# Kernel optimization log

Measured on AMD Instinct MI355X. Metric: run time of the kernel, lower is better.

## Reference

```python
import jax, jax.numpy as jnp
import numpy as np

B, T, D = 4, 2048, 1024
H, DK = 8, 64
EPS = 1e-6

def _xavier(key, shape):
    fan_in, fan_out = shape[1], shape[0]
    lim = float(np.sqrt(6.0 / (fan_in + fan_out)))
    return jax.random.uniform(key, shape, jnp.float32, -lim, lim)

def setup_inputs() -> dict:
    key = jax.random.key(0)
    ks = jax.random.split(key, 7)
    x = jax.random.normal(ks[0], (B, T, D), jnp.float32)
    W_Q = _xavier(ks[1], (H * DK, D))
    W_K = _xavier(ks[2], (H * DK, D))
    W_V = _xavier(ks[3], (H * DK, D))
    W_g_w = _xavier(ks[4], (H * DK, D))
    W_g_b = jax.random.normal(ks[5], (H * DK,), jnp.float32) * 0.02
    W_O = _xavier(ks[6], (D, H * DK))
    decay_log = jnp.zeros((H,), jnp.float32)
    return {"x": x, "W_Q": W_Q, "W_K": W_K, "W_V": W_V,
            "W_g_w": W_g_w, "W_g_b": W_g_b, "W_O": W_O,
            "decay_log": decay_log}

def _phi(u):
    # ELU + 1 feature map (positive)
    return jax.nn.elu(u) + 1.0

def reference(x, W_Q, W_K, W_V, W_g_w, W_g_b, W_O, decay_log):
    b, t, d = x.shape
    q = _phi((x @ W_Q.T).reshape(b, t, H, DK))
    k = _phi((x @ W_K.T).reshape(b, t, H, DK))
    v = (x @ W_V.T).reshape(b, t, H, DK)
    gamma = jax.nn.sigmoid(decay_log)           # [H]
    g4 = gamma[None, :, None, None]             # [1,H,1,1]
    g3 = gamma[None, :, None]                   # [1,H,1]

    # time-major for scan: [T,B,H,DK]
    qT = jnp.moveaxis(q, 1, 0)
    kT = jnp.moveaxis(k, 1, 0)
    vT = jnp.moveaxis(v, 1, 0)

    S0 = jnp.zeros((b, H, DK, DK), x.dtype)
    z0 = jnp.zeros((b, H, DK), x.dtype)

    def step(carry, inp):
        S, z = carry
        qt, kt, vt = inp
        S = g4 * S + jnp.einsum('bhi,bhj->bhij', kt, vt)
        z = g3 * z + kt
        num = jnp.einsum('bhij,bhi->bhj', S, qt)
        den = jnp.sum(z * qt, axis=-1, keepdims=True) + EPS
        return (S, z), num / den

    _, ys = jax.lax.scan(step, (S0, z0), (qT, kT, vT))  # ys: [T,B,H,DK]
    outputs = jnp.moveaxis(ys, 0, 1)                    # [B,T,H,DK]

    gate = jax.nn.sigmoid(x @ W_g_w.T + W_g_b).reshape(b, t, H, DK)
    y = (outputs * gate).reshape(b, t, H * DK)
    return y @ W_O.T
```

## Files before the change

kernel.cpp:

```cpp
#include <hip/hip_runtime.h>
#include <cstdint>
#include <cstddef>

#define B_   4
#define T_   2048
#define D_   1024
#define H_   8
#define DK_  64
#define HD_  512
#define CH_  64
#define NC_  32
#define EPS_ 1e-6f

typedef __attribute__((ext_vector_type(4))) float f32x4;
typedef __attribute__((ext_vector_type(8))) short s16x8;

__device__ __forceinline__ unsigned short f2bf(float f) {
    unsigned int x = __float_as_uint(f);
    unsigned int r = (x + 0x7FFFu + ((x >> 16) & 1u)) >> 16;
    return (unsigned short)r;
}
__device__ __forceinline__ float bf2f(unsigned short u) {
    return __uint_as_float(((unsigned int)u) << 16);
}
__device__ __forceinline__ void gl_lds16(const unsigned short* g, unsigned short* l) {
    __builtin_amdgcn_global_load_lds(
        (const __attribute__((address_space(1))) unsigned int*)g,
        (__attribute__((address_space(3))) unsigned int*)l, 16, 0, 0);
}

__global__ __launch_bounds__(256) void k_cvt_all(
    const float* __restrict__ x,
    const float* __restrict__ wq, const float* __restrict__ wk,
    const float* __restrict__ wv, const float* __restrict__ wgw,
    const float* __restrict__ wo,
    unsigned short* __restrict__ xb,
    unsigned short* __restrict__ wqb, unsigned short* __restrict__ wkb,
    unsigned short* __restrict__ wvb, unsigned short* __restrict__ wgb,
    unsigned short* __restrict__ wob)
{
    int bid = blockIdx.x;
    const float* src; unsigned short* dst; int idx;
    if (bid < 8192) {
        src = x; dst = xb; idx = bid * 256 + threadIdx.x;
    } else {
        int r = bid - 8192;
        int w = r >> 9;
        idx = (r & 511) * 256 + threadIdx.x;
        switch (w) {
            case 0:  src = wq;  dst = wqb; break;
            case 1:  src = wk;  dst = wkb; break;
            case 2:  src = wv;  dst = wvb; break;
            case 3:  src = wgw; dst = wgb; break;
            default: src = wo;  dst = wob; break;
        }
    }
    float4 v = ((const float4*)src)[idx];
    ushort4 o;
    o.x = f2bf(v.x); o.y = f2bf(v.y); o.z = f2bf(v.z); o.w = f2bf(v.w);
    ((ushort4*)dst)[idx] = o;
}

__global__ __launch_bounds__(512, 2) void k_gemm_qkvg(
    const unsigned short* __restrict__ xb,
    const unsigned short* __restrict__ wqb, const unsigned short* __restrict__ wkb,
    const unsigned short* __restrict__ wvb, const unsigned short* __restrict__ wgb,
    const float* __restrict__ bias,
    unsigned short* __restrict__ qo, unsigned short* __restrict__ ko,
    unsigned short* __restrict__ vo, unsigned short* __restrict__ go)
{
    __shared__ unsigned short As[2][256 * 64];
    __shared__ unsigned short Bs[2][256 * 64];
    const int tid = threadIdx.x;
    const int id  = blockIdx.x;
    const int xcd = id & 7, per = id >> 3;
    const int mtile = xcd * 4 + (per & 3);
    const int ntile = per >> 2;
    const int which = ntile >> 1;
    const int nb    = ntile & 1;
    const int m0    = mtile * 256;
    const int n0    = nb * 256;
    const unsigned short* Wp = (which == 0) ? wqb : (which == 1) ? wkb : (which == 2) ? wvb : wgb;
    unsigned short* Op       = (which == 0) ? qo  : (which == 1) ? ko  : (which == 2) ? vo  : go;
    const int K = D_;
    const int NIT = K / 64;

    const int lane = tid & 63, wave = tid >> 6;
    const int wm = (wave >> 2) * 128, wn = (wave & 3) * 64;
    const int r16 = lane & 15, quad = lane >> 4;
    const int lrow = lane >> 3, lseg = lane & 7;
    const int sseg = lseg ^ lrow;
    const int rx   = r16 & 7;

    f32x4 acc[8][4];
    #pragma unroll
    for (int a = 0; a < 8; a++)
        #pragma unroll
        for (int b = 0; b < 4; b++) acc[a][b] = 0.0f;

    auto stage = [&](int buf, int ko_) {
        #pragma unroll
        for (int i = 0; i < 4; i++) {
            int chunk = wave * 4 + i;
            int row = chunk * 8 + lrow;
            gl_lds16(xb + (size_t)(m0 + row) * K + ko_ + sseg * 8, &As[buf][chunk * 512]);
            gl_lds16(Wp + (size_t)(n0 + row) * K + ko_ + sseg * 8, &Bs[buf][chunk * 512]);
        }
    };

    stage(0, 0);
    for (int it = 0; it < NIT; ++it) {
        if (it + 1 < NIT) {
            stage((it + 1) & 1, (it + 1) * 64);
            asm volatile("s_waitcnt vmcnt(8)" ::: "memory");
        } else {
            asm volatile("s_waitcnt vmcnt(0)" ::: "memory");
        }
        __builtin_amdgcn_s_barrier();
        const int buf = it & 1;
        #pragma unroll
        for (int kk = 0; kk < 64; kk += 32) {
            const int gb_ = kk >> 3;
            s16x8 af[8], bf[4];
            #pragma unroll
            for (int mt = 0; mt < 8; mt++)
                af[mt] = *(const s16x8*)&As[buf][(wm + mt * 16 + r16) * 64 + (((gb_ + quad) ^ rx) << 3)];
            #pragma unroll
            for (int nt = 0; nt < 4; nt++)
                bf[nt] = *(const s16x8*)&Bs[buf][(wn + nt * 16 + r16) * 64 + (((gb_ + quad) ^ rx) << 3)];
            #pragma unroll
            for (int mt = 0; mt < 8; mt++)
                #pragma unroll
                for (int nt = 0; nt < 4; nt++)
                    acc[mt][nt] = __builtin_amdgcn_mfma_f32_16x16x32_bf16(af[mt], bf[nt], acc[mt][nt], 0, 0, 0);
        }
        __builtin_amdgcn_s_barrier();
    }
    #pragma unroll
    for (int mt = 0; mt < 8; mt++) {
        #pragma unroll
        for (int nt = 0; nt < 4; nt++) {
            int col = n0 + wn + nt * 16 + r16;
            float bv = (which == 3) ? bias[col] : 0.0f;
            #pragma unroll
            for (int r = 0; r < 4; r++) {
                int row = m0 + wm + mt * 16 + quad * 4 + r;
                float v = acc[mt][nt][r];
                if (which <= 1)      v = (v > 0.0f) ? v + 1.0f : __builtin_expf(v);
                else if (which == 3) v = 1.0f / (1.0f + __builtin_expf(-(v + bv)));
                Op[(size_t)row * HD_ + col] = f2bf(v);
            }
        }
    }
}

__global__ __launch_bounds__(512, 2) void k_gemm_out(
    const unsigned short* __restrict__ ogb, const unsigned short* __restrict__ wob,
    float* __restrict__ y)
{
    __shared__ unsigned short As[2][256 * 64];
    __shared__ unsigned short Bs[2][128 * 64];
    const int tid = threadIdx.x;
    const int id  = blockIdx.x;
    const int xcd = id & 7, per = id >> 3;
    const int m0 = (xcd * 4 + (per & 3)) * 256;
    const int n0 = (per >> 2) * 128;
    const int K = HD_;
    const int NIT = K / 64;

    const int lane = tid & 63, wave = tid >> 6;
    const int wm = (wave >> 1) * 64, wn = (wave & 1) * 64;
    const int r16 = lane & 15, quad = lane >> 4;
    const int lrow = lane >> 3, lseg = lane & 7;
    const int sseg = lseg ^ lrow;
    const int rx   = r16 & 7;

    f32x4 acc[4][4];
    #pragma unroll
    for (int a = 0; a < 4; a++)
        #pragma unroll
        for (int b = 0; b < 4; b++) acc[a][b] = 0.0f;

    auto stage = [&](int buf, int ko_) {
        #pragma unroll
        for (int i = 0; i < 4; i++) {
            int chunk = wave * 4 + i;
            int row = chunk * 8 + lrow;
            gl_lds16(ogb + (size_t)(m0 + row) * K + ko_ + sseg * 8, &As[buf][chunk * 512]);
        }
        #pragma unroll
        for (int i = 0; i < 2; i++) {
            int chunk = wave * 2 + i;
            int row = chunk * 8 + lrow;
            gl_lds16(wob + (size_t)(n0 + row) * K + ko_ + sseg * 8, &Bs[buf][chunk * 512]);
        }
    };

    stage(0, 0);
    for (int it = 0; it < NIT; ++it) {
        if (it + 1 < NIT) {
            stage((it + 1) & 1, (it + 1) * 64);
            asm volatile("s_waitcnt vmcnt(6)" ::: "memory");
        } else {
            asm volatile("s_waitcnt vmcnt(0)" ::: "memory");
        }
        __builtin_amdgcn_s_barrier();
        const int buf = it & 1;
        #pragma unroll
        for (int kk = 0; kk < 64; kk += 32) {
            const int gb_ = kk >> 3;
            s16x8 af[4], bf[4];
            #pragma unroll
            for (int mt = 0; mt < 4; mt++)
                af[mt] = *(const s16x8*)&As[buf][(wm + mt * 16 + r16) * 64 + (((gb_ + quad) ^ rx) << 3)];
            #pragma unroll
            for (int nt = 0; nt < 4; nt++)
                bf[nt] = *(const s16x8*)&Bs[buf][(wn + nt * 16 + r16) * 64 + (((gb_ + quad) ^ rx) << 3)];
            #pragma unroll
            for (int mt = 0; mt < 4; mt++)
                #pragma unroll
                for (int nt = 0; nt < 4; nt++)
                    acc[mt][nt] = __builtin_amdgcn_mfma_f32_16x16x32_bf16(af[mt], bf[nt], acc[mt][nt], 0, 0, 0);
        }
        __builtin_amdgcn_s_barrier();
    }
    #pragma unroll
    for (int mt = 0; mt < 4; mt++)
        #pragma unroll
        for (int nt = 0; nt < 4; nt++) {
            int col = n0 + wn + nt * 16 + r16;
            #pragma unroll
            for (int r = 0; r < 4; r++) {
                int row = m0 + wm + mt * 16 + quad * 4 + r;
                y[(size_t)row * D_ + col] = acc[mt][nt][r];
            }
        }
}

__global__ __launch_bounds__(256) void k_chunk_sums(
    const unsigned short* __restrict__ Kb, const unsigned short* __restrict__ Vb,
    float* __restrict__ Ssum, float* __restrict__ zsum, const float* __restrict__ decay_log)
{
    __shared__ unsigned short kt[64 * 72];
    __shared__ unsigned short vt[64 * 72];
    const int tid = threadIdx.x;
    const int bc  = blockIdx.x;
    const int c   = bc & (NC_ - 1);
    const int bh  = bc >> 5;
    const int h   = bh & (H_ - 1);
    const int b   = bh >> 3;
    const float g  = 1.0f / (1.0f + __builtin_expf(-decay_log[h]));
    const float lg = __builtin_log2f(g);
    const int t0 = c * CH_;

    #pragma unroll
    for (int e = 0; e < 2; e++) {
        int lid = e * 256 + tid;
        int l = lid >> 3, d0 = (lid & 7) * 8;
        float w = __builtin_exp2f((float)(CH_ - 1 - l) * lg);
        size_t gidx = (size_t)(b * T_ + t0 + l) * HD_ + h * DK_ + d0;
        uint4 kraw = *(const uint4*)(Kb + gidx);
        uint4 vraw = *(const uint4*)(Vb + gidx);
        const unsigned short* kp = (const unsigned short*)&kraw;
        const unsigned short* vp = (const unsigned short*)&vraw;
        #pragma unroll
        for (int j = 0; j < 8; j++) {
            kt[(d0 + j) * 72 + l] = f2bf(bf2f(kp[j]) * w);
            vt[(d0 + j) * 72 + l] = vp[j];
        }
    }
    __syncthreads();

    const int lane = tid & 63, wave = tid >> 6;
    const int r16 = lane & 15, quad = lane >> 4;
    size_t base = (size_t)bc * (DK_ * DK_);

    #pragma unroll
    for (int it = 0; it < 4; it++) {
        f32x4 sacc = 0.0f;
        #pragma unroll
        for (int ks = 0; ks < 2; ks++) {
            s16x8 af  = *(const s16x8*)&vt[(16 * wave + r16) * 72 + ks * 32 + quad * 8];
            s16x8 bf_ = *(const s16x8*)&kt[(16 * it   + r16) * 72 + ks * 32 + quad * 8];
            sacc = __builtin_amdgcn_mfma_f32_16x16x32_bf16(af, bf_, sacc, 0, 0, 0);
        }
        #pragma unroll
        for (int rr = 0; rr < 4; rr++)
            Ssum[base + (size_t)(16 * wave + quad * 4 + rr) * DK_ + 16 * it + r16] = sacc[rr];
    }
    if (tid < DK_) {
        float s = 0.0f;
        #pragma unroll
        for (int l8 = 0; l8 < 8; l8++) {
            uint4 kk = *(const uint4*)&kt[tid * 72 + l8 * 8];
            const unsigned short* kp = (const unsigned short*)&kk;
            #pragma unroll
            for (int e = 0; e < 8; e++) s += bf2f(kp[e]);
        }
        zsum[(size_t)bc * DK_ + tid] = s;
    }
}

__global__ __launch_bounds__(128) void k_chunk_scan(
    float* __restrict__ Ssum, float* __restrict__ zsum, const float* __restrict__ decay_log)
{
    const int tid = threadIdx.x;
    const int grp = blockIdx.x & 31;
    const int bh  = blockIdx.x >> 5;
    const int h   = bh & (H_ - 1);
    const float g  = 1.0f / (1.0f + __builtin_expf(-decay_log[h]));
    const float gC = __builtin_exp2f((float)CH_ * __builtin_log2f(g));
    int elem = grp * 128 + tid;
    float s = 0.0f;
    for (int c = 0; c < NC_; c++) {
        size_t idx = ((size_t)(bh * NC_ + c)) * 4096 + elem;
        float v = Ssum[idx];
        Ssum[idx] = s;
        s = gC * s + v;
    }
    if (grp == 0 && tid < DK_) {
        float z = 0.0f;
        for (int c = 0; c < NC_; c++) {
            size_t idx = ((size_t)(bh * NC_ + c)) * DK_ + tid;
            float v = zsum[idx];
            zsum[idx] = z;
            z = gC * z + v;
        }
    }
}

__global__ __launch_bounds__(256) void k_chunk_out(
    const unsigned short* __restrict__ Qb, const unsigned short* __restrict__ Kb,
    const unsigned short* __restrict__ Vb, const unsigned short* __restrict__ Gb,
    const float* __restrict__ Ssum, const float* __restrict__ zsum,
    unsigned short* __restrict__ OGb, const float* __restrict__ decay_log)
{
    __shared__ unsigned short ql[64 * 72];
    __shared__ unsigned short kl[64 * 72];
    __shared__ unsigned short sT[64 * 72];
    __shared__ unsigned short vt[64 * 72];
    __shared__ unsigned short pl[64 * 72];
    __shared__ float den_l[64];
    __shared__ float zp[64];
    __shared__ float gpow[CH_ + 1];

    const int tid = threadIdx.x;
    const int bc  = blockIdx.x;
    const int c   = bc & (NC_ - 1);
    const int bh  = bc >> 5;
    const int h   = bh & (H_ - 1);
    const int b   = bh >> 3;
    const float g  = 1.0f / (1.0f + __builtin_expf(-decay_log[h]));
    const float lg = __builtin_log2f(g);
    const int t0 = c * CH_;

    if (tid <= CH_) gpow[tid] = __builtin_exp2f((float)tid * lg);
    if (tid < DK_)  zp[tid] = zsum[(size_t)bc * DK_ + tid];

    #pragma unroll
    for (int e = 0; e < 2; e++) {
        int lid = e * 256 + tid;
        int l = lid >> 3, d0 = (lid & 7) * 8;
        size_t gidx = (size_t)(b * T_ + t0 + l) * HD_ + h * DK_ + d0;
        uint4 qraw = *(const uint4*)(Qb + gidx);
        uint4 kraw = *(const uint4*)(Kb + gidx);
        uint4 vraw = *(const uint4*)(Vb + gidx);
        *(uint4*)&ql[l * 72 + d0] = qraw;
        *(uint4*)&kl[l * 72 + d0] = kraw;
        const unsigned short* vp = (const unsigned short*)&vraw;
        #pragma unroll
        for (int j = 0; j < 8; j++) vt[(d0 + j) * 72 + l] = vp[j];
    }
    {
        int j = tid >> 2, seg = tid & 3;
        const float4* src = (const float4*)&Ssum[(size_t)bc * 4096 + (size_t)j * 64 + seg * 16];
        #pragma unroll
        for (int e = 0; e < 4; e++) {
            float4 a4 = src[e];
            ushort4 o;
            o.x = f2bf(a4.x); o.y = f2bf(a4.y); o.z = f2bf(a4.z); o.w = f2bf(a4.w);
            *(ushort4*)&sT[j * 72 + seg * 16 + e * 4] = o;
        }
    }
    __syncthreads();

    const int lane = tid & 63, wave = tid >> 6;
    const int r16 = lane & 15, quad = lane >> 4;
    const int ibase = 16 * wave;

    s16x8 aq[2];
    #pragma unroll
    for (int ks = 0; ks < 2; ks++)
        aq[ks] = *(const s16x8*)&ql[(ibase + r16) * 72 + ks * 32 + quad * 8];

    f32x4 sc4[4];
    #pragma unroll
    for (int lt = 0; lt < 4; lt++) {
        f32x4 s = 0.0f;
        #pragma unroll
        for (int ks = 0; ks < 2; ks++) {
            s16x8 bf_ = *(const s16x8*)&kl[(16 * lt + r16) * 72 + ks * 32 + quad * 8];
            s = __builtin_amdgcn_mfma_f32_16x16x32_bf16(aq[ks], bf_, s, 0, 0, 0);
        }
        sc4[lt] = s;
    }
    float rs[4] = {0.0f, 0.0f, 0.0f, 0.0f};
    #pragma unroll
    for (int lt = 0; lt < 4; lt++) {
        int l = 16 * lt + r16;
        #pragma unroll
        for (int rr = 0; rr < 4; rr++) {
            int i = ibase + quad * 4 + rr;
            float val = (l <= i) ? sc4[lt][rr] * gpow[i - l] : 0.0f;
            unsigned short pb = f2bf(val);
            pl[i * 72 + l] = pb;
            rs[rr] += bf2f(pb);
        }
    }
    #pragma unroll
    for (int rr = 0; rr < 4; rr++) {
        float v_ = rs[rr];
        v_ += __shfl_xor(v_, 1);
        v_ += __shfl_xor(v_, 2);
        v_ += __shfl_xor(v_, 4);
        v_ += __shfl_xor(v_, 8);
        if (r16 == 0) den_l[ibase + quad * 4 + rr] = v_;
    }
    f32x4 og[4];
    #pragma unroll
    for (int jt = 0; jt < 4; jt++) {
        f32x4 o = 0.0f;
        #pragma unroll
        for (int ks = 0; ks < 2; ks++) {
            s16x8 bf_ = *(const s16x8*)&sT[(16 * jt + r16) * 72 + ks * 32 + quad * 8];
            o = __builtin_amdgcn_mfma_f32_16x16x32_bf16(aq[ks], bf_, o, 0, 0, 0);
        }
        #pragma unroll
        for (int rr = 0; rr < 4; rr++)
            o[rr] *= gpow[ibase + quad * 4 + rr + 1];
        og[jt] = o;
    }
    __syncthreads();

    #pragma unroll
    for (int jt = 0; jt < 4; jt++) {
        #pragma unroll
        for (int ks = 0; ks < 2; ks++) {
            s16x8 ap  = *(const s16x8*)&pl[(ibase + r16) * 72 + ks * 32 + quad * 8];
            s16x8 bf_ = *(const s16x8*)&vt[(16 * jt + r16) * 72 + ks * 32 + quad * 8];
            og[jt] = __builtin_amdgcn_mfma_f32_16x16x32_bf16(ap, bf_, og[jt], 0, 0, 0);
        }
    }
    if (tid < DK_) {
        float dp = 0.0f;
        #pragma unroll
        for (int d8 = 0; d8 < 8; d8++) {
            uint4 qq = *(const uint4*)&ql[tid * 72 + d8 * 8];
            const unsigned short* qp = (const unsigned short*)&qq;
            #pragma unroll
            for (int e = 0; e < 8; e++) dp += bf2f(qp[e]) * zp[d8 * 8 + e];
        }
        den_l[tid] += gpow[tid + 1] * dp + EPS_;
    }
    __syncthreads();

    #pragma unroll
    for (int jt = 0; jt < 4; jt++) {
        int j = 16 * jt + r16;
        #pragma unroll
        for (int rr = 0; rr < 4; rr++) {
            int i = ibase + quad * 4 + rr;
            float rcp = 1.0f / den_l[i];
            size_t ga = (size_t)(b * T_ + t0 + i) * HD_ + h * DK_ + j;
            float gate = bf2f(Gb[ga]);
            OGb[ga] = f2bf(og[jt][rr] * rcp * gate);
        }
    }
}

extern "C" void kernel_launch(void* const* d_in, const int* in_sizes, int n_in,
                              void* d_out, int out_size, void* d_ws, size_t ws_size,
                              hipStream_t stream)
{
    (void)in_sizes; (void)n_in; (void)out_size; (void)ws_size;
    const float* x         = (const float*)d_in[0];
    const float* W_Q       = (const float*)d_in[1];
    const float* W_K       = (const float*)d_in[2];
    const float* W_V       = (const float*)d_in[3];
    const float* W_gw      = (const float*)d_in[4];
    const float* W_gb      = (const float*)d_in[5];
    const float* W_O       = (const float*)d_in[6];
    const float* decay_log = (const float*)d_in[7];
    float* y = (float*)d_out;

    char* ws = (char*)d_ws;
    size_t off = 0;
    auto alloc = [&](size_t bytes) { void* p = ws + off; off += (bytes + 255) & ~(size_t)255; return p; };
    unsigned short* xb   = (unsigned short*)alloc((size_t)B_ * T_ * D_ * 2);
    unsigned short* wqb  = (unsigned short*)alloc((size_t)HD_ * D_ * 2);
    unsigned short* wkb  = (unsigned short*)alloc((size_t)HD_ * D_ * 2);
    unsigned short* wvb  = (unsigned short*)alloc((size_t)HD_ * D_ * 2);
    unsigned short* wgb  = (unsigned short*)alloc((size_t)HD_ * D_ * 2);
    unsigned short* wob  = (unsigned short*)alloc((size_t)D_ * HD_ * 2);
    unsigned short* qb   = (unsigned short*)alloc((size_t)B_ * T_ * HD_ * 2);
    unsigned short* kb   = (unsigned short*)alloc((size_t)B_ * T_ * HD_ * 2);
    unsigned short* vb   = (unsigned short*)alloc((size_t)B_ * T_ * HD_ * 2);
    unsigned short* gb   = (unsigned short*)alloc((size_t)B_ * T_ * HD_ * 2);
    unsigned short* ogb  = (unsigned short*)alloc((size_t)B_ * T_ * HD_ * 2);
    float* Ssum = (float*)alloc((size_t)B_ * H_ * NC_ * DK_ * DK_ * 4);
    float* zsum = (float*)alloc((size_t)B_ * H_ * NC_ * DK_ * 4);

    k_cvt_all<<<8192 + 5 * 512, 256, 0, stream>>>(x, W_Q, W_K, W_V, W_gw, W_O,
                                                  xb, wqb, wkb, wvb, wgb, wob);
    k_gemm_qkvg<<<256, 512, 0, stream>>>(xb, wqb, wkb, wvb, wgb, W_gb, qb, kb, vb, gb);
    k_chunk_sums<<<B_ * H_ * NC_, 256, 0, stream>>>(kb, vb, Ssum, zsum, decay_log);
    k_chunk_scan<<<B_ * H_ * NC_, 128, 0, stream>>>(Ssum, zsum, decay_log);
    k_chunk_out<<<B_ * H_ * NC_, 256, 0, stream>>>(qb, kb, vb, gb, Ssum, zsum, ogb, decay_log);
    k_gemm_out<<<256, 512, 0, stream>>>(ogb, wob, y);
}
```

Before: 197.9 us.

## Fuse chunk sums, scan, and output into one cooperative kernel with grid syncs

Merges the three chunked linear-attention kernels into a single cooperative launch of 512 blocks, each handling two chunks, separated by grid-wide syncs. The scan phase spreads across all threads of the grid. This removes two kernel launches and their inter-kernel gaps, at the cost of grid.sync overhead and a grid limited to co-resident blocks (two per CU via launch bounds).

New measurement: 442.7 us. 124% more time.

```diff
diff --git a/kernel.cpp b/kernel.cpp
--- a/kernel.cpp
+++ b/kernel.cpp
@@ -1,6 +1,9 @@
 #include <hip/hip_runtime.h>
+#include <hip/hip_cooperative_groups.h>
 #include <cstdint>
 #include <cstddef>
+
+namespace cg = cooperative_groups;
 
 #define B_   4
 #define T_   2048
@@ -237,243 +240,247 @@
         }
 }
 
-__global__ __launch_bounds__(256) void k_chunk_sums(
-    const unsigned short* __restrict__ Kb, const unsigned short* __restrict__ Vb,
-    float* __restrict__ Ssum, float* __restrict__ zsum, const float* __restrict__ decay_log)
+__global__ __launch_bounds__(256, 2) void k_chunk_all(
+    const unsigned short* __restrict__ Qb, const unsigned short* __restrict__ Kb,
+    const unsigned short* __restrict__ Vb, const unsigned short* __restrict__ Gb,
+    float* __restrict__ Ssum, float* __restrict__ zsum,
+    unsigned short* __restrict__ OGb, const float* __restrict__ decay_log)
 {
     __shared__ unsigned short kt[64 * 72];
     __shared__ unsigned short vt[64 * 72];
-    const int tid = threadIdx.x;
-    const int bc  = blockIdx.x;
-    const int c   = bc & (NC_ - 1);
-    const int bh  = bc >> 5;
-    const int h   = bh & (H_ - 1);
-    const int b   = bh >> 3;
-    const float g  = 1.0f / (1.0f + __builtin_expf(-decay_log[h]));
-    const float lg = __builtin_log2f(g);
-    const int t0 = c * CH_;
-
-    #pragma unroll
-    for (int e = 0; e < 2; e++) {
-        int lid = e * 256 + tid;
-        int l = lid >> 3, d0 = (lid & 7) * 8;
-        float w = __builtin_exp2f((float)(CH_ - 1 - l) * lg);
-        size_t gidx = (size_t)(b * T_ + t0 + l) * HD_ + h * DK_ + d0;
-        uint4 kraw = *(const uint4*)(Kb + gidx);
-        uint4 vraw = *(const uint4*)(Vb + gidx);
-        const unsigned short* kp = (const unsigned short*)&kraw;
-        const unsigned short* vp = (const unsigned short*)&vraw;
-        #pragma unroll
-        for (int j = 0; j < 8; j++) {
-            kt[(d0 + j) * 72 + l] = f2bf(bf2f(kp[j]) * w);
-            vt[(d0 + j) * 72 + l] = vp[j];
-        }
-    }
-    __syncthreads();
-
-    const int lane = tid & 63, wave = tid >> 6;
-    const int r16 = lane & 15, quad = lane >> 4;
-    size_t base = (size_t)bc * (DK_ * DK_);
-
-    #pragma unroll
-    for (int it = 0; it < 4; it++) {
-        f32x4 sacc = 0.0f;
-        #pragma unroll
-        for (int ks = 0; ks < 2; ks++) {
-            s16x8 af  = *(const s16x8*)&vt[(16 * wave + r16) * 72 + ks * 32 + quad * 8];
-            s16x8 bf_ = *(const s16x8*)&kt[(16 * it   + r16) * 72 + ks * 32 + quad * 8];
-            sacc = __builtin_amdgcn_mfma_f32_16x16x32_bf16(af, bf_, sacc, 0, 0, 0);
-        }
-        #pragma unroll
-        for (int rr = 0; rr < 4; rr++)
-            Ssum[base + (size_t)(16 * wave + quad * 4 + rr) * DK_ + 16 * it + r16] = sacc[rr];
-    }
-    if (tid < DK_) {
-        float s = 0.0f;
-        #pragma unroll
-        for (int l8 = 0; l8 < 8; l8++) {
-            uint4 kk = *(const uint4*)&kt[tid * 72 + l8 * 8];
-            const unsigned short* kp = (const unsigned short*)&kk;
-            #pragma unroll
-            for (int e = 0; e < 8; e++) s += bf2f(kp[e]);
-        }
-        zsum[(size_t)bc * DK_ + tid] = s;
-    }
-}
-
-__global__ __launch_bounds__(128) void k_chunk_scan(
-    float* __restrict__ Ssum, float* __restrict__ zsum, const float* __restrict__ decay_log)
-{
-    const int tid = threadIdx.x;
-    const int grp = blockIdx.x & 31;
-    const int bh  = blockIdx.x >> 5;
-    const int h   = bh & (H_ - 1);
-    const float g  = 1.0f / (1.0f + __builtin_expf(-decay_log[h]));
-    const float gC = __builtin_exp2f((float)CH_ * __builtin_log2f(g));
-    int elem = grp * 128 + tid;
-    float s = 0.0f;
-    for (int c = 0; c < NC_; c++) {
-        size_t idx = ((size_t)(bh * NC_ + c)) * 4096 + elem;
-        float v = Ssum[idx];
-        Ssum[idx] = s;
-        s = gC * s + v;
-    }
-    if (grp == 0 && tid < DK_) {
-        float z = 0.0f;
-        for (int c = 0; c < NC_; c++) {
-            size_t idx = ((size_t)(bh * NC_ + c)) * DK_ + tid;
-            float v = zsum[idx];
-            zsum[idx] = z;
-            z = gC * z + v;
-        }
-    }
-}
-
-__global__ __launch_bounds__(256) void k_chunk_out(
-    const unsigned short* __restrict__ Qb, const unsigned short* __restrict__ Kb,
-    const unsigned short* __restrict__ Vb, const unsigned short* __restrict__ Gb,
-    const float* __restrict__ Ssum, const float* __restrict__ zsum,
-    unsigned short* __restrict__ OGb, const float* __restrict__ decay_log)
-{
     __shared__ unsigned short ql[64 * 72];
     __shared__ unsigned short kl[64 * 72];
     __shared__ unsigned short sT[64 * 72];
-    __shared__ unsigned short vt[64 * 72];
     __shared__ unsigned short pl[64 * 72];
     __shared__ float den_l[64];
     __shared__ float zp[64];
     __shared__ float gpow[CH_ + 1];
 
     const int tid = threadIdx.x;
-    const int bc  = blockIdx.x;
-    const int c   = bc & (NC_ - 1);
-    const int bh  = bc >> 5;
-    const int h   = bh & (H_ - 1);
-    const int b   = bh >> 3;
-    const float g  = 1.0f / (1.0f + __builtin_expf(-decay_log[h]));
-    const float lg = __builtin_log2f(g);
-    const int t0 = c * CH_;
-
-    if (tid <= CH_) gpow[tid] = __builtin_exp2f((float)tid * lg);
-    if (tid < DK_)  zp[tid] = zsum[(size_t)bc * DK_ + tid];
-
-    #pragma unroll
-    for (int e = 0; e < 2; e++) {
-        int lid = e * 256 + tid;
-        int l = lid >> 3, d0 = (lid & 7) * 8;
-        size_t gidx = (size_t)(b * T_ + t0 + l) * HD_ + h * DK_ + d0;
-        uint4 qraw = *(const uint4*)(Qb + gidx);
-        uint4 kraw = *(const uint4*)(Kb + gidx);
-        uint4 vraw = *(const uint4*)(Vb + gidx);
-        *(uint4*)&ql[l * 72 + d0] = qraw;
-        *(uint4*)&kl[l * 72 + d0] = kraw;
-        const unsigned short* vp = (const unsigned short*)&vraw;
-        #pragma unroll
-        for (int j = 0; j < 8; j++) vt[(d0 + j) * 72 + l] = vp[j];
-    }
-    {
-        int j = tid >> 2, seg = tid & 3;
-        const float4* src = (const float4*)&Ssum[(size_t)bc * 4096 + (size_t)j * 64 + seg * 16];
-        #pragma unroll
-        for (int e = 0; e < 4; e++) {
-            float4 a4 = src[e];
-            ushort4 o;
-            o.x = f2bf(a4.x); o.y = f2bf(a4.y); o.z = f2bf(a4.z); o.w = f2bf(a4.w);
-            *(ushort4*)&sT[j * 72 + seg * 16 + e * 4] = o;
-        }
-    }
-    __syncthreads();
-
     const int lane = tid & 63, wave = tid >> 6;
     const int r16 = lane & 15, quad = lane >> 4;
-    const int ibase = 16 * wave;
-
-    s16x8 aq[2];
-    #pragma unroll
-    for (int ks = 0; ks < 2; ks++)
-        aq[ks] = *(const s16x8*)&ql[(ibase + r16) * 72 + ks * 32 + quad * 8];
-
-    f32x4 sc4[4];
-    #pragma unroll
-    for (int lt = 0; lt < 4; lt++) {
-        f32x4 s = 0.0f;
-        #pragma unroll
-        for (int ks = 0; ks < 2; ks++) {
-            s16x8 bf_ = *(const s16x8*)&kl[(16 * lt + r16) * 72 + ks * 32 + quad * 8];
-            s = __builtin_amdgcn_mfma_f32_16x16x32_bf16(aq[ks], bf_, s, 0, 0, 0);
-        }
-        sc4[lt] = s;
-    }
-    float rs[4] = {0.0f, 0.0f, 0.0f, 0.0f};
-    #pragma unroll
-    for (int lt = 0; lt < 4; lt++) {
-        int l = 16 * lt + r16;
+    cg::grid_group grid = cg::this_grid();
+
+    for (int rep = 0; rep < 2; ++rep) {
+        if (rep) __syncthreads();
+        const int bc = blockIdx.x + rep * 512;
+        const int c   = bc & (NC_ - 1);
+        const int bh  = bc >> 5;
+        const int h   = bh & (H_ - 1);
+        const int b   = bh >> 3;
+        const float g  = 1.0f / (1.0f + __builtin_expf(-decay_log[h]));
+        const float lg = __builtin_log2f(g);
+        const int t0 = c * CH_;
+
+        #pragma unroll
+        for (int e = 0; e < 2; e++) {
+            int lid = e * 256 + tid;
+            int l = lid >> 3, d0 = (lid & 7) * 8;
+            float w = __builtin_exp2f((float)(CH_ - 1 - l) * lg);
+            size_t gidx = (size_t)(b * T_ + t0 + l) * HD_ + h * DK_ + d0;
+            uint4 kraw = *(const uint4*)(Kb + gidx);
+            uint4 vraw = *(const uint4*)(Vb + gidx);
+            const unsigned short* kp = (const unsigned short*)&kraw;
+            const unsigned short* vp = (const unsigned short*)&vraw;
+            #pragma unroll
+            for (int j = 0; j < 8; j++) {
+                kt[(d0 + j) * 72 + l] = f2bf(bf2f(kp[j]) * w);
+                vt[(d0 + j) * 72 + l] = vp[j];
+            }
+        }
+        __syncthreads();
+
+        size_t base = (size_t)bc * (DK_ * DK_);
+        #pragma unroll
+        for (int it = 0; it < 4; it++) {
+            f32x4 sacc = 0.0f;
+            #pragma unroll
+            for (int ks = 0; ks < 2; ks++) {
+                s16x8 af  = *(const s16x8*)&vt[(16 * wave + r16) * 72 + ks * 32 + quad * 8];
+                s16x8 bf_ = *(const s16x8*)&kt[(16 * it   + r16) * 72 + ks * 32 + quad * 8];
+                sacc = __builtin_amdgcn_mfma_f32_16x16x32_bf16(af, bf_, sacc, 0, 0, 0);
+            }
+            #pragma unroll
+            for (int rr = 0; rr < 4; rr++)
+                Ssum[base + (size_t)(16 * wave + quad * 4 + rr) * DK_ + 16 * it + r16] = sacc[rr];
+        }
+        if (tid < DK_) {
+            float s = 0.0f;
+            #pragma unroll
+            for (int l8 = 0; l8 < 8; l8++) {
+                uint4 kk = *(const uint4*)&kt[tid * 72 + l8 * 8];
+                const unsigned short* kp = (const unsigned short*)&kk;
+                #pragma unroll
+                for (int e = 0; e < 8; e++) s += bf2f(kp[e]);
+            }
+            zsum[(size_t)bc * DK_ + tid] = s;
+        }
+    }
+
+    __threadfence();
+    grid.sync();
+
+    {
+        int id = blockIdx.x * 256 + tid;
+        int bh = id >> 12;
+        int elem = id & 4095;
+        const int h = bh & (H_ - 1);
+        const float g  = 1.0f / (1.0f + __builtin_expf(-decay_log[h]));
+        const float gC = __builtin_exp2f((float)CH_ * __builtin_log2f(g));
+        float s = 0.0f;
+        for (int c = 0; c < NC_; c++) {
+            size_t idx = ((size_t)(bh * NC_ + c)) * 4096 + elem;
+            float v = Ssum[idx];
+            Ssum[idx] = s;
+            s = gC * s + v;
+        }
+        if (id < 32 * DK_) {
+            int zbh = id >> 6, zelem = id & 63;
+            const int zh = zbh & (H_ - 1);
+            const float zg  = 1.0f / (1.0f + __builtin_expf(-decay_log[zh]));
+            const float zgC = __builtin_exp2f((float)CH_ * __builtin_log2f(zg));
+            float z = 0.0f;
+            for (int c = 0; c < NC_; c++) {
+                size_t idx = ((size_t)(zbh * NC_ + c)) * DK_ + zelem;
+                float v = zsum[idx];
+                zsum[idx] = z;
+                z = zgC * z + v;
+            }
+        }
+    }
+
+    __threadfence();
+    grid.sync();
+
+    for (int rep = 0; rep < 2; ++rep) {
+        __syncthreads();
+        const int bc = blockIdx.x + rep * 512;
+        const int c   = bc & (NC_ - 1);
+        const int bh  = bc >> 5;
+        const int h   = bh & (H_ - 1);
+        const int b   = bh >> 3;
+        const float g  = 1.0f / (1.0f + __builtin_expf(-decay_log[h]));
+        const float lg = __builtin_log2f(g);
+        const int t0 = c * CH_;
+
+        if (tid <= CH_) gpow[tid] = __builtin_exp2f((float)tid * lg);
+        if (tid < DK_)  zp[tid] = zsum[(size_t)bc * DK_ + tid];
+
+        #pragma unroll
+        for (int e = 0; e < 2; e++) {
+            int lid = e * 256 + tid;
+            int l = lid >> 3, d0 = (lid & 7) * 8;
+            size_t gidx = (size_t)(b * T_ + t0 + l) * HD_ + h * DK_ + d0;
+            uint4 qraw = *(const uint4*)(Qb + gidx);
+            uint4 kraw = *(const uint4*)(Kb + gidx);
+            uint4 vraw = *(const uint4*)(Vb + gidx);
+            *(uint4*)&ql[l * 72 + d0] = qraw;
+            *(uint4*)&kl[l * 72 + d0] = kraw;
+            const unsigned short* vp = (const unsigned short*)&vraw;
+            #pragma unroll
+            for (int j = 0; j < 8; j++) vt[(d0 + j) * 72 + l] = vp[j];
+        }
+        {
+            int j = tid >> 2, seg = tid & 3;
+            const float4* src = (const float4*)&Ssum[(size_t)bc * 4096 + (size_t)j * 64 + seg * 16];
+            #pragma unroll
+            for (int e = 0; e < 4; e++) {
+                float4 a4 = src[e];
+                ushort4 o;
+                o.x = f2bf(a4.x); o.y = f2bf(a4.y); o.z = f2bf(a4.z); o.w = f2bf(a4.w);
+                *(ushort4*)&sT[j * 72 + seg * 16 + e * 4] = o;
+            }
+        }
+        __syncthreads();
+
+        const int ibase = 16 * wave;
+        s16x8 aq[2];
+        #pragma unroll
+        for (int ks = 0; ks < 2; ks++)
+            aq[ks] = *(const s16x8*)&ql[(ibase + r16) * 72 + ks * 32 + quad * 8];
+
+        f32x4 sc4[4];
+        #pragma unroll
+        for (int lt = 0; lt < 4; lt++) {
+            f32x4 s = 0.0f;
+            #pragma unroll
+            for (int ks = 0; ks < 2; ks++) {
+                s16x8 bf_ = *(const s16x8*)&kl[(16 * lt + r16) * 72 + ks * 32 + quad * 8];
+                s = __builtin_amdgcn_mfma_f32_16x16x32_bf16(aq[ks], bf_, s, 0, 0, 0);
+            }
+            sc4[lt] = s;
+        }
+        float rs[4] = {0.0f, 0.0f, 0.0f, 0.0f};
+        #pragma unroll
+        for (int lt = 0; lt < 4; lt++) {
+            int l = 16 * lt + r16;
+            #pragma unroll
+            for (int rr = 0; rr < 4; rr++) {
+                int i = ibase + quad * 4 + rr;
+                float val = (l <= i) ? sc4[lt][rr] * gpow[i - l] : 0.0f;
+                unsigned short pb = f2bf(val);
+                pl[i * 72 + l] = pb;
+                rs[rr] += bf2f(pb);
+            }
+        }
         #pragma unroll
         for (int rr = 0; rr < 4; rr++) {
-            int i = ibase + quad * 4 + rr;
-            float val = (l <= i) ? sc4[lt][rr] * gpow[i - l] : 0.0f;
-            unsigned short pb = f2bf(val);
-            pl[i * 72 + l] = pb;
-            rs[rr] += bf2f(pb);
-        }
-    }
-    #pragma unroll
-    for (int rr = 0; rr < 4; rr++) {
-        float v_ = rs[rr];
-        v_ += __shfl_xor(v_, 1);
-        v_ += __shfl_xor(v_, 2);
-        v_ += __shfl_xor(v_, 4);
-        v_ += __shfl_xor(v_, 8);
-        if (r16 == 0) den_l[ibase + quad * 4 + rr] = v_;
-    }
-    f32x4 og[4];
-    #pragma unroll
-    for (int jt = 0; jt < 4; jt++) {
-        f32x4 o = 0.0f;
-        #pragma unroll
-        for (int ks = 0; ks < 2; ks++) {
-            s16x8 bf_ = *(const s16x8*)&sT[(16 * jt + r16) * 72 + ks * 32 + quad * 8];
-            o = __builtin_amdgcn_mfma_f32_16x16x32_bf16(aq[ks], bf_, o, 0, 0, 0);
-        }
-        #pragma unroll
-        for (int rr = 0; rr < 4; rr++)
-            o[rr] *= gpow[ibase + quad * 4 + rr + 1];
-        og[jt] = o;
-    }
-    __syncthreads();
-
-    #pragma unroll
-    for (int jt = 0; jt < 4; jt++) {
-        #pragma unroll
-        for (int ks = 0; ks < 2; ks++) {
-            s16x8 ap  = *(const s16x8*)&pl[(ibase + r16) * 72 + ks * 32 + quad * 8];
-            s16x8 bf_ = *(const s16x8*)&vt[(16 * jt + r16) * 72 + ks * 32 + quad * 8];
-            og[jt] = __builtin_amdgcn_mfma_f32_16x16x32_bf16(ap, bf_, og[jt], 0, 0, 0);
-        }
-    }
-    if (tid < DK_) {
-        float dp = 0.0f;
-        #pragma unroll
-        for (int d8 = 0; d8 < 8; d8++) {
-            uint4 qq = *(const uint4*)&ql[tid * 72 + d8 * 8];
-            const unsigned short* qp = (const unsigned short*)&qq;
-            #pragma unroll
-            for (int e = 0; e < 8; e++) dp += bf2f(qp[e]) * zp[d8 * 8 + e];
-        }
-        den_l[tid] += gpow[tid + 1] * dp + EPS_;
-    }
-    __syncthreads();
-
-    #pragma unroll
-    for (int jt = 0; jt < 4; jt++) {
-        int j = 16 * jt + r16;
-        #pragma unroll
-        for (int rr = 0; rr < 4; rr++) {
-            int i = ibase + quad * 4 + rr;
-            float rcp = 1.0f / den_l[i];
-            size_t ga = (size_t)(b * T_ + t0 + i) * HD_ + h * DK_ + j;
-            float gate = bf2f(Gb[ga]);
-            OGb[ga] = f2bf(og[jt][rr] * rcp * gate);
+            float v_ = rs[rr];
+            v_ += __shfl_xor(v_, 1);
+            v_ += __shfl_xor(v_, 2);
+            v_ += __shfl_xor(v_, 4);
+            v_ += __shfl_xor(v_, 8);
+            if (r16 == 0) den_l[ibase + quad * 4 + rr] = v_;
+        }
+        f32x4 og[4];
+        #pragma unroll
+        for (int jt = 0; jt < 4; jt++) {
+            f32x4 o = 0.0f;
+            #pragma unroll
+            for (int ks = 0; ks < 2; ks++) {
+                s16x8 bf_ = *(const s16x8*)&sT[(16 * jt + r16) * 72 + ks * 32 + quad * 8];
+                o = __builtin_amdgcn_mfma_f32_16x16x32_bf16(aq[ks], bf_, o, 0, 0, 0);
+            }
+            #pragma unroll
+            for (int rr = 0; rr < 4; rr++)
+                o[rr] *= gpow[ibase + quad * 4 + rr + 1];
+            og[jt] = o;
+        }
+        __syncthreads();
+
+        #pragma unroll
+        for (int jt = 0; jt < 4; jt++) {
+            #pragma unroll
+            for (int ks = 0; ks < 2; ks++) {
+                s16x8 ap  = *(const s16x8*)&pl[(ibase + r16) * 72 + ks * 32 + quad * 8];
+                s16x8 bf_ = *(const s16x8*)&vt[(16 * jt + r16) * 72 + ks * 32 + quad * 8];
+                og[jt] = __builtin_amdgcn_mfma_f32_16x16x32_bf16(ap, bf_, og[jt], 0, 0, 0);
+            }
+        }
+        if (tid < DK_) {
+            float dp = 0.0f;
+            #pragma unroll
+            for (int d8 = 0; d8 < 8; d8++) {
+                uint4 qq = *(const uint4*)&ql[tid * 72 + d8 * 8];
+                const unsigned short* qp = (const unsigned short*)&qq;
+                #pragma unroll
+                for (int e = 0; e < 8; e++) dp += bf2f(qp[e]) * zp[d8 * 8 + e];
+            }
+            den_l[tid] += gpow[tid + 1] * dp + EPS_;
+        }
+        __syncthreads();
+
+        #pragma unroll
+        for (int jt = 0; jt < 4; jt++) {
+            int j = 16 * jt + r16;
+            #pragma unroll
+            for (int rr = 0; rr < 4; rr++) {
+                int i = ibase + quad * 4 + rr;
+                float rcp = 1.0f / den_l[i];
+                size_t ga = (size_t)(b * T_ + t0 + i) * HD_ + h * DK_ + j;
+                float gate = bf2f(Gb[ga]);
+                OGb[ga] = f2bf(og[jt][rr] * rcp * gate);
+            }
         }
     }
 }
@@ -513,8 +520,13 @@
     k_cvt_all<<<8192 + 5 * 512, 256, 0, stream>>>(x, W_Q, W_K, W_V, W_gw, W_O,
                                                   xb, wqb, wkb, wvb, wgb, wob);
     k_gemm_qkvg<<<256, 512, 0, stream>>>(xb, wqb, wkb, wvb, wgb, W_gb, qb, kb, vb, gb);
-    k_chunk_sums<<<B_ * H_ * NC_, 256, 0, stream>>>(kb, vb, Ssum, zsum, decay_log);
-    k_chunk_scan<<<B_ * H_ * NC_, 128, 0, stream>>>(Ssum, zsum, decay_log);
-    k_chunk_out<<<B_ * H_ * NC_, 256, 0, stream>>>(qb, kb, vb, gb, Ssum, zsum, ogb, decay_log);
+
+    {
+        void* args[] = { (void*)&qb, (void*)&kb, (void*)&vb, (void*)&gb,
+                         (void*)&Ssum, (void*)&zsum, (void*)&ogb, (void*)&decay_log };
+        hipLaunchCooperativeKernel((const void*)k_chunk_all, dim3(512), dim3(256),
+                                   args, 0, stream);
+    }
+
     k_gemm_out<<<256, 512, 0, stream>>>(ogb, wob, y);
 }
```
